# Optimization experiments

Measured on AMD Instinct MI355X. Metric: run time of the kernel, lower is better.

Reference implementation:

```python
import jax, jax.numpy as jnp
import numpy as np

LN_EPS = 1e-5


def setup_inputs() -> dict:
    key = jax.random.key(0)
    ks = jax.random.split(key, 10)
    B, T, S, C = 8, 1024, 2048, 1024
    sd = 1.0 / np.sqrt(C)
    return {
        "x": jax.random.normal(ks[0], (B, T, C), jnp.float32),
        "lfb_feats": jax.random.normal(ks[1], (B, S, C), jnp.float32),
        "theta_w": jax.random.normal(ks[2], (C, C), jnp.float32) * sd,
        "theta_b": jax.random.normal(ks[3], (C,), jnp.float32) * 0.01,
        "phi_w": jax.random.normal(ks[4], (C, C), jnp.float32) * sd,
        "phi_b": jax.random.normal(ks[5], (C,), jnp.float32) * 0.01,
        "gi_w": jax.random.normal(ks[6], (C, C), jnp.float32) * sd,
        "gi_b": jax.random.normal(ks[7], (C,), jnp.float32) * 0.01,
        "ln_g": jnp.ones((C,), jnp.float32),
        "ln_b": jnp.zeros((C,), jnp.float32),
        "fc_w": jax.random.normal(ks[8], (C, C), jnp.float32) * sd,
        "fc_b": jax.random.normal(ks[9], (C,), jnp.float32) * 0.01,
    }


def _layernorm(h, g, b):
    mu = jnp.mean(h, axis=-1, keepdims=True)
    var = jnp.var(h, axis=-1, keepdims=True)
    return (h - mu) * jax.lax.rsqrt(var + LN_EPS) * g + b


def reference(x, lfb_feats, theta_w, theta_b, phi_w, phi_b, gi_w, gi_b,
              ln_g, ln_b, fc_w, fc_b):
    # x: [B,T,C], lfb_feats: [B,S,C]. 1x1 Conv1d == per-token linear on channels.
    C = x.shape[-1]
    scale = jnp.sqrt(jnp.asarray(C, x.dtype))  # NOTE: 1/sqrt(1/C) = sqrt(C) (as in source)
    theta = jnp.einsum('btc,oc->bto', x, theta_w) + theta_b          # [B,T,C]
    phi = jnp.einsum('bsc,oc->bso', lfb_feats, phi_w) + phi_b        # [B,S,C]
    gi = jnp.einsum('bsc,oc->bso', lfb_feats, gi_w) + gi_b           # [B,S,C]
    attn = jax.nn.softmax(jnp.einsum('btc,bsc->bts', theta, phi) * scale, axis=-1)
    out = jnp.einsum('bts,bsc->btc', attn, gi)                       # [B,T,C]
    out = jax.nn.relu(_layernorm(out, ln_g, ln_b))
    out = jnp.einsum('btc,oc->bto', out, fc_w) + fc_b                # fc (dropout = identity at eval)
    return out + x                                                   # residual, [B,T,C]
```

## Files before the change

### kernel.cpp

```cpp
#include <hip/hip_runtime.h>


#define BM 128
#define BN 128
#define BK 64

typedef __attribute__((ext_vector_type(8))) short short8;
typedef __attribute__((ext_vector_type(4))) float f32x4;
typedef __attribute__((ext_vector_type(4))) unsigned short us4;

enum { MODE_SPLIT = 0, MODE_TRANS = 1, MODE_F32 = 2, MODE_FINAL = 3 };

__device__ __forceinline__ float b2f(unsigned short u) {
  union { unsigned int i; float f; } x;
  x.i = ((unsigned int)u) << 16;
  return x.f;
}
__device__ __forceinline__ unsigned short f2b(float f) {
  unsigned int u = __float_as_uint(f);
  unsigned int r = (u + 0x7FFFu + ((u >> 16) & 1u)) >> 16;
  return (unsigned short)r;
}

__device__ __forceinline__ void async_cp16(const unsigned short* g,
                                           unsigned short* l) {
  __builtin_amdgcn_global_load_lds(
      (const __attribute__((address_space(1))) void*)g,
      (__attribute__((address_space(3))) void*)l, 16, 0, 0);
}

__global__ __launch_bounds__(256) void split_hilo(const float* __restrict__ src,
                                                  unsigned short* __restrict__ dst,
                                                  int n4) {
  int g = blockIdx.x * 256 + threadIdx.x;
  if (g >= n4) return;
  const int e = g * 4;
  const int r = e >> 10;
  const int c = e & 1023;
  f32x4 v = *(const f32x4*)&src[e];
  us4 hi, lo;
#pragma unroll
  for (int i = 0; i < 4; ++i) {
    hi[i] = f2b(v[i]);
    lo[i] = f2b(v[i] - b2f(hi[i]));
  }
  *(us4*)&dst[(size_t)r * 2048 + c] = hi;
  *(us4*)&dst[(size_t)r * 2048 + 1024 + c] = lo;
}

__global__ __launch_bounds__(256) void split_lfb_v(
    const float* __restrict__ lfb, const float* __restrict__ g,
    unsigned short* __restrict__ ls, float* __restrict__ v) {
  const int row = blockIdx.x;
  const int t = threadIdx.x;
  const int c = t * 4;
  __shared__ float red[4];
  f32x4 x = *(const f32x4*)&lfb[(size_t)row * 1024 + c];
  f32x4 gg = *(const f32x4*)&g[c];
  us4 hi, lo;
  float s = 0.f;
#pragma unroll
  for (int i = 0; i < 4; ++i) {
    hi[i] = f2b(x[i]);
    lo[i] = f2b(x[i] - b2f(hi[i]));
    s += x[i] * gg[i];
  }
  *(us4*)&ls[(size_t)row * 2048 + c] = hi;
  *(us4*)&ls[(size_t)row * 2048 + 1024 + c] = lo;
  for (int o = 32; o; o >>= 1) s += __shfl_xor(s, o, 64);
  if ((t & 63) == 0) red[t >> 6] = s;
  __syncthreads();
  if (t == 0) v[row] = red[0] + red[1] + red[2] + red[3];
}

__global__ __launch_bounds__(256) void cvt2_bf16(const float* __restrict__ s0,
                                                 unsigned short* __restrict__ d0,
                                                 const float* __restrict__ s1,
                                                 unsigned short* __restrict__ d1) {
  int b = blockIdx.x;
  const float* src = (b < 1024) ? s0 : s1;
  unsigned short* dst = (b < 1024) ? d0 : d1;
  int g = (b & 1023) * 256 + threadIdx.x;
  f32x4 v = *(const f32x4*)&src[g * 4];
  us4 o;
#pragma unroll
  for (int i = 0; i < 4; ++i) o[i] = f2b(v[i]);
  *(us4*)&dst[(size_t)g * 4] = o;
}

__global__ __launch_bounds__(256) void transpose_split(
    const float* __restrict__ W, unsigned short* __restrict__ T) {
  __shared__ float tile[64][65];
  const int bo = blockIdx.y * 64;
  const int bc = blockIdx.x * 64;
  const int t = threadIdx.x;
  const int tr = t >> 4;
  const int tc = (t & 15) * 4;
#pragma unroll
  for (int i = 0; i < 4; ++i) {
    f32x4 v = *(const f32x4*)&W[(size_t)(bo + tr + 16 * i) * 1024 + bc + tc];
#pragma unroll
    for (int j = 0; j < 4; ++j) tile[tr + 16 * i][tc + j] = v[j];
  }
  __syncthreads();
#pragma unroll
  for (int i = 0; i < 4; ++i) {
    const int c = bc + tr + 16 * i;
    us4 hi, lo;
#pragma unroll
    for (int j = 0; j < 4; ++j) {
      float v = tile[tc + j][tr + 16 * i];
      hi[j] = f2b(v);
      lo[j] = f2b(v - b2f(hi[j]));
    }
    *(us4*)&T[(size_t)c * 2048 + bo + tc] = hi;
    *(us4*)&T[(size_t)c * 2048 + 1024 + bo + tc] = lo;
  }
}

__global__ __launch_bounds__(256) void make_g(
    const unsigned short* __restrict__ tB, const float* __restrict__ bth,
    float* __restrict__ g) {
  const int d = blockIdx.x * 4 + (threadIdx.x >> 6);
  const int lane = threadIdx.x & 63;
  float s = 0.f;
#pragma unroll
  for (int i = 0; i < 4; ++i) {
    const int o0 = lane * 4 + i * 256;
    us4 h = *(const us4*)&tB[(size_t)d * 2048 + o0];
    us4 lo = *(const us4*)&tB[(size_t)d * 2048 + 1024 + o0];
    f32x4 bb = *(const f32x4*)&bth[o0];
#pragma unroll
    for (int j = 0; j < 4; ++j) s += (b2f(h[j]) + b2f(lo[j])) * bb[j];
  }
  for (int o = 32; o; o >>= 1) s += __shfl_xor(s, o, 64);
  if (lane == 0) g[d] = s;
}

template <int MODE>
__global__ __launch_bounds__(256, 2) void gemm_bt(
    const unsigned short* __restrict__ A, const unsigned short* __restrict__ B,
    void* __restrict__ Cout, const float* __restrict__ bias,
    const float* __restrict__ resid, int M, int N, int K, int lda, int ldb,
    int ldc, long long sA, long long sB, long long sC, long long sBias,
    int awrap, int awoff, int bwrap, int bwoff, int NBk, int MBk, int mbx,
    int swz) {
  __shared__ __align__(16) unsigned short As[BM * BK];
  __shared__ __align__(16) unsigned short Bs[BN * BK];

  const int tid = threadIdx.x;
  const int l = tid & 63;
  const int w = tid >> 6;
  const int wm = w >> 1, wn = w & 1;
  const int ln = l & 15, lq = l >> 4;

  int bmi, bni, bzi;
  {
    const int id = blockIdx.x;
    if (swz == 1) {
      bzi = id & 7;
      const int r = id >> 3;
      bmi = r % mbx;
      bni = r / mbx;
    } else if (swz == 2) {
      bzi = 0;
      const int r = id >> 3;
      bmi = (id & 7) * mbx + r % mbx;
      bni = r / mbx;
    } else {
      bni = id % NBk;
      const int rem = id / NBk;
      bmi = rem % MBk;
      bzi = rem / MBk;
    }
  }
  const int bm = bmi * BM;
  const int bn = bni * BN;
  const unsigned short* Ab = A + (size_t)bzi * (size_t)sA;
  const unsigned short* Bb = B + (size_t)bzi * (size_t)sB;
  const float* bz = bias ? bias + (size_t)bzi * (size_t)sBias : nullptr;

  const int arow = tid >> 3;
  const int acol = (((tid & 7) ^ ((tid >> 3) & 7)) * 8);
  const int ldsbase = (tid & 0xC0) * 8;

  f32x4 acc[4][4];
#pragma unroll
  for (int i = 0; i < 4; ++i)
#pragma unroll
    for (int j = 0; j < 4; ++j) acc[i][j] = (f32x4){0.f, 0.f, 0.f, 0.f};

  const int sw = ln & 7;

  for (int k0 = 0; k0 < K; k0 += BK) {
    const int ka = (k0 < awrap) ? k0 : k0 - awoff;
    const int kb = (k0 < bwrap) ? k0 : k0 - bwoff;
#pragma unroll
    for (int it = 0; it < 4; ++it) {
      const int r = it * 32 + arow;
      async_cp16(Ab + (size_t)(bm + r) * lda + ka + acol,
                 &As[it * 2048 + ldsbase]);
    }
#pragma unroll
    for (int it = 0; it < 4; ++it) {
      const int r = it * 32 + arow;
      async_cp16(Bb + (size_t)(bn + r) * ldb + kb + acol,
                 &Bs[it * 2048 + ldsbase]);
    }
    __syncthreads();

#pragma unroll
    for (int ks = 0; ks < 2; ++ks) {
      short8 a[4], b[4];
      const int kof = ((ks * 4 + lq) ^ sw) * 8;
#pragma unroll
      for (int i = 0; i < 4; ++i)
        a[i] = *(const short8*)&As[(wm * 64 + i * 16 + ln) * BK + kof];
#pragma unroll
      for (int j = 0; j < 4; ++j)
        b[j] = *(const short8*)&Bs[(wn * 64 + j * 16 + ln) * BK + kof];
#pragma unroll
      for (int i = 0; i < 4; ++i)
#pragma unroll
        for (int j = 0; j < 4; ++j)
          acc[i][j] = __builtin_amdgcn_mfma_f32_16x16x32_bf16(a[i], b[j],
                                                              acc[i][j], 0, 0, 0);
    }
    __syncthreads();
  }

  float* Cf = (float*)Cout + (size_t)bzi * (size_t)sC;
  unsigned short* Cb = (unsigned short*)Cout + (size_t)bzi * (size_t)sC;

  if constexpr (MODE == MODE_TRANS) {
#pragma unroll
    for (int i = 0; i < 4; ++i) {
      const int gm0 = bm + wm * 64 + i * 16 + lq * 4;
      const int bt = gm0 >> 11;
      const int sr = gm0 & 2047;
#pragma unroll
      for (int j = 0; j < 4; ++j) {
        const int gn = bn + wn * 64 + j * 16 + ln;
        const float bv2 = (bz != nullptr) ? bz[gn] : 0.f;
        us4 o;
#pragma unroll
        for (int r = 0; r < 4; ++r) o[r] = f2b(acc[i][j][r] + bv2);
        *(us4*)&Cb[(size_t)bt * 2097152 + (size_t)gn * 2048 + sr] = o;
      }
    }
  } else {
#pragma unroll
    for (int j = 0; j < 4; ++j) {
      const int gn = bn + wn * 64 + j * 16 + ln;
      const float bv2 = (bz != nullptr) ? bz[gn] : 0.f;
#pragma unroll
      for (int i = 0; i < 4; ++i) {
        const int gm0 = bm + wm * 64 + i * 16 + lq * 4;
#pragma unroll
        for (int r = 0; r < 4; ++r) {
          const int gm = gm0 + r;
          const float v = acc[i][j][r] + bv2;
          if constexpr (MODE == MODE_SPLIT) {
            unsigned short hi = f2b(v);
            Cb[(size_t)gm * ldc + gn] = hi;
            Cb[(size_t)gm * ldc + gn + (ldc >> 1)] = f2b(v - b2f(hi));
          } else if constexpr (MODE == MODE_F32) {
            Cf[(size_t)gm * ldc + gn] = v;
          } else if constexpr (MODE == MODE_FINAL) {
            const size_t idx = (size_t)gm * ldc + gn;
            Cf[idx] = v + resid[idx];
          }
        }
      }
    }
  }
}

__global__ __launch_bounds__(256) void softmax_rows(
    const float* __restrict__ logit, unsigned short* __restrict__ attn) {
  const int row = blockIdx.x;
  const float* L = logit + (size_t)row * 2048;
  unsigned short* O = attn + (size_t)row * 2048;
  const int t = threadIdx.x;
  __shared__ float red[8];

  f32x4 v0 = *(const f32x4*)&L[t * 4];
  f32x4 v1 = *(const f32x4*)&L[t * 4 + 1024];
  float m = fmaxf(fmaxf(fmaxf(v0[0], v0[1]), fmaxf(v0[2], v0[3])),
                  fmaxf(fmaxf(v1[0], v1[1]), fmaxf(v1[2], v1[3])));
  for (int o = 32; o; o >>= 1) m = fmaxf(m, __shfl_xor(m, o, 64));
  if ((t & 63) == 0) red[t >> 6] = m;
  __syncthreads();
  m = fmaxf(fmaxf(red[0], red[1]), fmaxf(red[2], red[3]));

  float e[8];
  float s = 0.f;
#pragma unroll
  for (int i = 0; i < 4; ++i) { e[i] = __expf(32.f * (v0[i] - m)); s += e[i]; }
#pragma unroll
  for (int i = 0; i < 4; ++i) { e[4 + i] = __expf(32.f * (v1[i] - m)); s += e[4 + i]; }
  for (int o = 32; o; o >>= 1) s += __shfl_xor(s, o, 64);
  if ((t & 63) == 0) red[4 + (t >> 6)] = s;
  __syncthreads();
  s = red[4] + red[5] + red[6] + red[7];
  const float inv = 1.f / s;
  us4 o0, o1;
#pragma unroll
  for (int i = 0; i < 4; ++i) { o0[i] = f2b(e[i] * inv); o1[i] = f2b(e[4 + i] * inv); }
  *(us4*)&O[t * 4] = o0;
  *(us4*)&O[t * 4 + 1024] = o1;
}

__global__ __launch_bounds__(256) void ln_relu(
    const float* __restrict__ X, const float* __restrict__ g,
    const float* __restrict__ b, unsigned short* __restrict__ H) {
  const int row = blockIdx.x;
  const float* x = X + (size_t)row * 1024;
  unsigned short* h = H + (size_t)row * 1024;
  const int t = threadIdx.x;
  __shared__ float red[8];
  f32x4 v = *(const f32x4*)&x[t * 4];
  float s = v[0] + v[1] + v[2] + v[3];
  float q = v[0] * v[0] + v[1] * v[1] + v[2] * v[2] + v[3] * v[3];
  for (int o = 32; o; o >>= 1) {
    s += __shfl_xor(s, o, 64);
    q += __shfl_xor(q, o, 64);
  }
  if ((t & 63) == 0) { red[t >> 6] = s; red[4 + (t >> 6)] = q; }
  __syncthreads();
  s = red[0] + red[1] + red[2] + red[3];
  q = red[4] + red[5] + red[6] + red[7];
  const float mean = s * (1.f / 1024.f);
  const float var = q * (1.f / 1024.f) - mean * mean;
  const float rstd = rsqrtf(var + 1e-5f);
  us4 o;
#pragma unroll
  for (int i = 0; i < 4; ++i) {
    const int c = t * 4 + i;
    const float y = (v[i] - mean) * rstd * g[c] + b[c];
    o[i] = f2b(fmaxf(y, 0.f));
  }
  *(us4*)&h[t * 4] = o;
}

extern "C" void kernel_launch(void* const* d_in, const int* in_sizes, int n_in,
                              void* d_out, int out_size, void* d_ws,
                              size_t ws_size, hipStream_t stream) {
  const float* x = (const float*)d_in[0];
  const float* lfb = (const float*)d_in[1];
  const float* th_w = (const float*)d_in[2];
  const float* th_b = (const float*)d_in[3];
  const float* ph_w = (const float*)d_in[4];
  const float* gi_w = (const float*)d_in[6];
  const float* gi_b = (const float*)d_in[7];
  const float* lng = (const float*)d_in[8];
  const float* lnb = (const float*)d_in[9];
  const float* fc_w = (const float*)d_in[10];
  const float* fc_b = (const float*)d_in[11];
  float* outf = (float*)d_out;
  char* ws = (char*)d_ws;

  const size_t MB = 1048576;
  int nb = 1;
  for (int cand = 8; cand >= 1; cand >>= 1)
    if ((size_t)cand * 24 * MB + 18 * MB <= ws_size) { nb = cand; break; }

  char* tail = ws + (size_t)nb * 24 * MB;
  unsigned short* tA = (unsigned short*)(tail);
  unsigned short* tB = (unsigned short*)(tail + 4 * MB);
  unsigned short* Gs = (unsigned short*)(tail + 8 * MB);
  unsigned short* giw = (unsigned short*)(tail + 12 * MB);
  unsigned short* fcw = (unsigned short*)(tail + 14 * MB);
  float* gv = (float*)(tail + 16 * MB);
  float* vb = (float*)(tail + 16 * MB + 65536);

  dim3 blk(256);
  transpose_split<<<dim3(16, 16), blk, 0, stream>>>(th_w, tA);
  transpose_split<<<dim3(16, 16), blk, 0, stream>>>(ph_w, tB);
  make_g<<<dim3(256), blk, 0, stream>>>(tB, th_b, gv);
  gemm_bt<MODE_SPLIT><<<dim3(64), blk, 0, stream>>>(
      tB, tA, Gs, nullptr, nullptr, 1024, 1024, 3072, 2048, 2048, 2048,
      0, 0, 0, 0, 2048, 2048, 1024, 1024, 8, 8, 1, 2);
  cvt2_bf16<<<dim3(2048), blk, 0, stream>>>(gi_w, giw, fc_w, fcw);

  for (int b0 = 0; b0 < 8; b0 += nb) {
    unsigned short* xs = (unsigned short*)(ws);
    float* logit = (float*)(ws);
    unsigned short* ls = (unsigned short*)(ws + (size_t)nb * 8 * MB);
    unsigned short* ys = (unsigned short*)(ws + (size_t)nb * 16 * MB);
    unsigned short* giT = (unsigned short*)(ws + (size_t)nb * 20 * MB);
    unsigned short* attn = ys;
    float* outp = (float*)ws;
    unsigned short* h = giT;

    const float* xb = x + (size_t)b0 * 1048576;
    const float* lfbb = lfb + (size_t)b0 * 2097152;
    float* ob = outf + (size_t)b0 * 1048576;
    const int Ms = nb * 2048;
    const int Mt = nb * 1024;
    const int zswz = (nb == 8) ? 1 : 0;

    split_lfb_v<<<dim3(Ms), blk, 0, stream>>>(lfbb, gv, ls, vb);
    gemm_bt<MODE_TRANS><<<dim3(8 * (Ms / 128)), blk, 0, stream>>>(
        ls, giw, giT, gi_b, nullptr, Ms, 1024, 1024, 2048, 1024, 2048,
        0, 0, 0, 0, 1024, 0, 1024, 0, 8, Ms / 128, Ms / 1024, 2);
    split_hilo<<<dim3(Mt), blk, 0, stream>>>(xb, xs, Mt * 256);
    gemm_bt<MODE_SPLIT><<<dim3(8 * (Mt / 128)), blk, 0, stream>>>(
        xs, Gs, ys, nullptr, nullptr, Mt, 1024, 3072, 2048, 2048, 2048,
        0, 0, 0, 0, 2048, 2048, 1024, 1024, 8, Mt / 128, Mt / 1024, 2);
    gemm_bt<MODE_F32><<<dim3(16 * 8 * nb), blk, 0, stream>>>(
        ys, ls, logit, vb, nullptr, 1024, 2048, 3072, 2048, 2048, 2048,
        2097152LL, 4194304LL, 2097152LL, 2048LL, 2048, 2048, 1024, 1024,
        16, 8, 8, zswz);
    softmax_rows<<<dim3(Mt), blk, 0, stream>>>(logit, attn);
    gemm_bt<MODE_F32><<<dim3(8 * 8 * nb), blk, 0, stream>>>(
        attn, giT, outp, nullptr, nullptr, 1024, 1024, 2048, 2048, 2048, 1024,
        2097152LL, 2097152LL, 1048576LL, 0, 2048, 0, 2048, 0, 8, 8, 8, zswz);
    ln_relu<<<dim3(Mt), blk, 0, stream>>>(outp, lng, lnb, h);
    gemm_bt<MODE_FINAL><<<dim3(8 * (Mt / 128)), blk, 0, stream>>>(
        h, fcw, ob, fc_b, xb, Mt, 1024, 1024, 1024, 1024, 1024,
        0, 0, 0, 0, 1024, 0, 1024, 0, 8, Mt / 128, Mt / 1024, 2);
  }
}
```

Measured before the change: 556.9 us.

## Split-K the weight-product GEMM, merge split kernels, raise GEMM occupancy

The precomputed theta/phi weight product GEMM used only 64 blocks. It is now split along K into 8 partial GEMMs (512 blocks) whose outputs a new kernel sums and splits into hi/lo bf16. The two transpose kernels are merged into one launch, and the lfb and x split kernels are merged into one. The GEMM launch bound min-blocks rises from 2 to 4, which may force register spilling in the 4x4 accumulator tiles. These changes target launch overhead and underutilisation in the small setup stages, at the cost of an extra fp32 partial buffer round trip.

Result: faster. 515.8 us (-7.4%).

```diff
diff --git a/kernel.cpp b/kernel.cpp
--- a/kernel.cpp
+++ b/kernel.cpp
@@ -29,48 +29,43 @@
       (__attribute__((address_space(3))) void*)l, 16, 0, 0);
 }
 
-__global__ __launch_bounds__(256) void split_hilo(const float* __restrict__ src,
-                                                  unsigned short* __restrict__ dst,
-                                                  int n4) {
-  int g = blockIdx.x * 256 + threadIdx.x;
-  if (g >= n4) return;
-  const int e = g * 4;
-  const int r = e >> 10;
-  const int c = e & 1023;
-  f32x4 v = *(const f32x4*)&src[e];
-  us4 hi, lo;
-#pragma unroll
-  for (int i = 0; i < 4; ++i) {
-    hi[i] = f2b(v[i]);
-    lo[i] = f2b(v[i] - b2f(hi[i]));
-  }
-  *(us4*)&dst[(size_t)r * 2048 + c] = hi;
-  *(us4*)&dst[(size_t)r * 2048 + 1024 + c] = lo;
-}
-
-__global__ __launch_bounds__(256) void split_lfb_v(
-    const float* __restrict__ lfb, const float* __restrict__ g,
-    unsigned short* __restrict__ ls, float* __restrict__ v) {
-  const int row = blockIdx.x;
+__global__ __launch_bounds__(256) void split_xlfb(
+    const float* __restrict__ lfb, const float* __restrict__ x,
+    const float* __restrict__ g, unsigned short* __restrict__ ls,
+    unsigned short* __restrict__ xs, float* __restrict__ v, int Ms) {
+  const int id = blockIdx.x;
   const int t = threadIdx.x;
   const int c = t * 4;
-  __shared__ float red[4];
-  f32x4 x = *(const f32x4*)&lfb[(size_t)row * 1024 + c];
-  f32x4 gg = *(const f32x4*)&g[c];
-  us4 hi, lo;
-  float s = 0.f;
-#pragma unroll
-  for (int i = 0; i < 4; ++i) {
-    hi[i] = f2b(x[i]);
-    lo[i] = f2b(x[i] - b2f(hi[i]));
-    s += x[i] * gg[i];
-  }
-  *(us4*)&ls[(size_t)row * 2048 + c] = hi;
-  *(us4*)&ls[(size_t)row * 2048 + 1024 + c] = lo;
-  for (int o = 32; o; o >>= 1) s += __shfl_xor(s, o, 64);
-  if ((t & 63) == 0) red[t >> 6] = s;
-  __syncthreads();
-  if (t == 0) v[row] = red[0] + red[1] + red[2] + red[3];
+  if (id < Ms) {
+    __shared__ float red[4];
+    f32x4 xv = *(const f32x4*)&lfb[(size_t)id * 1024 + c];
+    f32x4 gg = *(const f32x4*)&g[c];
+    us4 hi, lo;
+    float s = 0.f;
+#pragma unroll
+    for (int i = 0; i < 4; ++i) {
+      hi[i] = f2b(xv[i]);
+      lo[i] = f2b(xv[i] - b2f(hi[i]));
+      s += xv[i] * gg[i];
+    }
+    *(us4*)&ls[(size_t)id * 2048 + c] = hi;
+    *(us4*)&ls[(size_t)id * 2048 + 1024 + c] = lo;
+    for (int o = 32; o; o >>= 1) s += __shfl_xor(s, o, 64);
+    if ((t & 63) == 0) red[t >> 6] = s;
+    __syncthreads();
+    if (t == 0) v[id] = red[0] + red[1] + red[2] + red[3];
+  } else {
+    const int r = id - Ms;
+    f32x4 xv = *(const f32x4*)&x[(size_t)r * 1024 + c];
+    us4 hi, lo;
+#pragma unroll
+    for (int i = 0; i < 4; ++i) {
+      hi[i] = f2b(xv[i]);
+      lo[i] = f2b(xv[i] - b2f(hi[i]));
+    }
+    *(us4*)&xs[(size_t)r * 2048 + c] = hi;
+    *(us4*)&xs[(size_t)r * 2048 + 1024 + c] = lo;
+  }
 }
 
 __global__ __launch_bounds__(256) void cvt2_bf16(const float* __restrict__ s0,
@@ -88,10 +83,14 @@
   *(us4*)&dst[(size_t)g * 4] = o;
 }
 
-__global__ __launch_bounds__(256) void transpose_split(
-    const float* __restrict__ W, unsigned short* __restrict__ T) {
+__global__ __launch_bounds__(256) void transpose_split2(
+    const float* __restrict__ W0, unsigned short* __restrict__ T0,
+    const float* __restrict__ W1, unsigned short* __restrict__ T1) {
   __shared__ float tile[64][65];
-  const int bo = blockIdx.y * 64;
+  const int sel = blockIdx.y >> 4;
+  const float* W = sel ? W1 : W0;
+  unsigned short* T = sel ? T1 : T0;
+  const int bo = (blockIdx.y & 15) * 64;
   const int bc = blockIdx.x * 64;
   const int t = threadIdx.x;
   const int tr = t >> 4;
@@ -137,14 +136,35 @@
   if (lane == 0) g[d] = s;
 }
 
+__global__ __launch_bounds__(256) void reduce_g(const float* __restrict__ P,
+                                                unsigned short* __restrict__ Gs) {
+  const int d = blockIdx.x;
+  const int c = threadIdx.x * 4;
+  f32x4 s = *(const f32x4*)&P[(size_t)d * 1024 + c];
+#pragma unroll
+  for (int z = 1; z < 8; ++z) {
+    f32x4 p = *(const f32x4*)&P[(size_t)z * 1048576 + (size_t)d * 1024 + c];
+#pragma unroll
+    for (int i = 0; i < 4; ++i) s[i] += p[i];
+  }
+  us4 hi, lo;
+#pragma unroll
+  for (int i = 0; i < 4; ++i) {
+    hi[i] = f2b(s[i]);
+    lo[i] = f2b(s[i] - b2f(hi[i]));
+  }
+  *(us4*)&Gs[(size_t)d * 2048 + c] = hi;
+  *(us4*)&Gs[(size_t)d * 2048 + 1024 + c] = lo;
+}
+
 template <int MODE>
-__global__ __launch_bounds__(256, 2) void gemm_bt(
+__global__ __launch_bounds__(256, 4) void gemm_bt(
     const unsigned short* __restrict__ A, const unsigned short* __restrict__ B,
     void* __restrict__ Cout, const float* __restrict__ bias,
     const float* __restrict__ resid, int M, int N, int K, int lda, int ldb,
     int ldc, long long sA, long long sB, long long sC, long long sBias,
     int awrap, int awoff, int bwrap, int bwoff, int NBk, int MBk, int mbx,
-    int swz) {
+    int swz, int kzoff) {
   __shared__ __align__(16) unsigned short As[BM * BK];
   __shared__ __align__(16) unsigned short Bs[BN * BK];
 
@@ -179,6 +199,7 @@
   const unsigned short* Ab = A + (size_t)bzi * (size_t)sA;
   const unsigned short* Bb = B + (size_t)bzi * (size_t)sB;
   const float* bz = bias ? bias + (size_t)bzi * (size_t)sBias : nullptr;
+  const int kbase = bzi * kzoff;
 
   const int arow = tid >> 3;
   const int acol = (((tid & 7) ^ ((tid >> 3) & 7)) * 8);
@@ -193,8 +214,9 @@
   const int sw = ln & 7;
 
   for (int k0 = 0; k0 < K; k0 += BK) {
-    const int ka = (k0 < awrap) ? k0 : k0 - awoff;
-    const int kb = (k0 < bwrap) ? k0 : k0 - bwoff;
+    const int kg = k0 + kbase;
+    const int ka = (kg < awrap) ? kg : kg - awoff;
+    const int kb = (kg < bwrap) ? kg : kg - bwoff;
 #pragma unroll
     for (int it = 0; it < 4; ++it) {
       const int r = it * 32 + arow;
@@ -375,12 +397,19 @@
   float* vb = (float*)(tail + 16 * MB + 65536);
 
   dim3 blk(256);
-  transpose_split<<<dim3(16, 16), blk, 0, stream>>>(th_w, tA);
-  transpose_split<<<dim3(16, 16), blk, 0, stream>>>(ph_w, tB);
+  transpose_split2<<<dim3(16, 32), blk, 0, stream>>>(th_w, tA, ph_w, tB);
   make_g<<<dim3(256), blk, 0, stream>>>(tB, th_b, gv);
-  gemm_bt<MODE_SPLIT><<<dim3(64), blk, 0, stream>>>(
-      tB, tA, Gs, nullptr, nullptr, 1024, 1024, 3072, 2048, 2048, 2048,
-      0, 0, 0, 0, 2048, 2048, 1024, 1024, 8, 8, 1, 2);
+  if (nb >= 2) {
+    float* gpart = (float*)ws;
+    gemm_bt<MODE_F32><<<dim3(512), blk, 0, stream>>>(
+        tB, tA, gpart, nullptr, nullptr, 1024, 1024, 384, 2048, 2048, 1024,
+        0, 0, 1048576LL, 0, 2048, 2048, 1024, 1024, 8, 8, 8, 1, 384);
+    reduce_g<<<dim3(1024), blk, 0, stream>>>(gpart, Gs);
+  } else {
+    gemm_bt<MODE_SPLIT><<<dim3(64), blk, 0, stream>>>(
+        tB, tA, Gs, nullptr, nullptr, 1024, 1024, 3072, 2048, 2048, 2048,
+        0, 0, 0, 0, 2048, 2048, 1024, 1024, 8, 8, 1, 2, 0);
+  }
   cvt2_bf16<<<dim3(2048), blk, 0, stream>>>(gi_w, giw, fc_w, fcw);
 
   for (int b0 = 0; b0 < 8; b0 += nb) {
@@ -400,25 +429,24 @@
     const int Mt = nb * 1024;
     const int zswz = (nb == 8) ? 1 : 0;
 
-    split_lfb_v<<<dim3(Ms), blk, 0, stream>>>(lfbb, gv, ls, vb);
+    split_xlfb<<<dim3(Ms + Mt), blk, 0, stream>>>(lfbb, xb, gv, ls, xs, vb, Ms);
     gemm_bt<MODE_TRANS><<<dim3(8 * (Ms / 128)), blk, 0, stream>>>(
         ls, giw, giT, gi_b, nullptr, Ms, 1024, 1024, 2048, 1024, 2048,
-        0, 0, 0, 0, 1024, 0, 1024, 0, 8, Ms / 128, Ms / 1024, 2);
-    split_hilo<<<dim3(Mt), blk, 0, stream>>>(xb, xs, Mt * 256);
+        0, 0, 0, 0, 1024, 0, 1024, 0, 8, Ms / 128, Ms / 1024, 2, 0);
     gemm_bt<MODE_SPLIT><<<dim3(8 * (Mt / 128)), blk, 0, stream>>>(
         xs, Gs, ys, nullptr, nullptr, Mt, 1024, 3072, 2048, 2048, 2048,
-        0, 0, 0, 0, 2048, 2048, 1024, 1024, 8, Mt / 128, Mt / 1024, 2);
+        0, 0, 0, 0, 2048, 2048, 1024, 1024, 8, Mt / 128, Mt / 1024, 2, 0);
     gemm_bt<MODE_F32><<<dim3(16 * 8 * nb), blk, 0, stream>>>(
         ys, ls, logit, vb, nullptr, 1024, 2048, 3072, 2048, 2048, 2048,
         2097152LL, 4194304LL, 2097152LL, 2048LL, 2048, 2048, 1024, 1024,
-        16, 8, 8, zswz);
+        16, 8, 8, zswz, 0);
     softmax_rows<<<dim3(Mt), blk, 0, stream>>>(logit, attn);
     gemm_bt<MODE_F32><<<dim3(8 * 8 * nb), blk, 0, stream>>>(
         attn, giT, outp, nullptr, nullptr, 1024, 1024, 2048, 2048, 2048, 1024,
-        2097152LL, 2097152LL, 1048576LL, 0, 2048, 0, 2048, 0, 8, 8, 8, zswz);
+        2097152LL, 2097152LL, 1048576LL, 0, 2048, 0, 2048, 0, 8, 8, 8, zswz, 0);
     ln_relu<<<dim3(Mt), blk, 0, stream>>>(outp, lng, lnb, h);
     gemm_bt<MODE_FINAL><<<dim3(8 * (Mt / 128)), blk, 0, stream>>>(
         h, fcw, ob, fc_b, xb, Mt, 1024, 1024, 1024, 1024, 1024,
-        0, 0, 0, 0, 1024, 0, 1024, 0, 8, Mt / 128, Mt / 1024, 2);
-  }
-}
+        0, 0, 0, 0, 1024, 0, 1024, 0, 8, Mt / 128, Mt / 1024, 2, 0);
+  }
+}
```
